# Performance work log

Hardware: AMD Instinct MI355X
Metric: run time of the kernel (lower is better)

Reference implementation:

```python
import jax, jax.numpy as jnp
import numpy as np

H = 16       # query heads
KV = 4       # key/value heads
HD = 256     # head dim
ROPE_THETA = 10000.0
EPS = 1e-6


def _rms_norm(x, w):
    # Gemma RMSNorm over last dim: x / rms * (1 + w), computed in fp32
    xf = x.astype(jnp.float32)
    var = jnp.mean(xf * xf, axis=-1, keepdims=True)
    out = xf * jax.lax.rsqrt(var + EPS) * (1.0 + w.astype(jnp.float32))
    return out.astype(x.dtype)


def _rope_cos_sin(position_ids):
    # cos/sin tables of shape [S, HD]
    inv_freq = 1.0 / (ROPE_THETA ** (jnp.arange(0, HD, 2, dtype=jnp.float32) / HD))
    ang = position_ids.astype(jnp.float32)[:, None] * inv_freq[None, :]  # [S, HD/2]
    emb = jnp.concatenate([ang, ang], axis=-1)                           # [S, HD]
    return jnp.cos(emb), jnp.sin(emb)


def _rotate_half(x):
    x1, x2 = jnp.split(x, 2, axis=-1)
    return jnp.concatenate([-x2, x1], axis=-1)


def _apply_rope(x, cos, sin):
    # x: [B, h, S, HD]; cos/sin: [S, HD] -> broadcast over batch and heads
    c = cos[None, None, :, :]
    s = sin[None, None, :, :]
    return (x * c + _rotate_half(x) * s).astype(x.dtype)


def setup_inputs() -> dict:
    key = jax.random.key(0)
    ks = jax.random.split(key, 8)
    B, S, D = 2, 2048, 2048
    inp = {
        "hidden_states": jax.random.normal(ks[0], (B, S, D), jnp.float32),
        "Wq": jax.random.normal(ks[1], (D, H * HD), jnp.float32) * 0.02,
        "Wk": jax.random.normal(ks[2], (D, KV * HD), jnp.float32) * 0.02,
        "Wv": jax.random.normal(ks[3], (D, KV * HD), jnp.float32) * 0.02,
        "Wo": jax.random.normal(ks[4], (H * HD, D), jnp.float32) * 0.02,
        "q_norm_w": jnp.zeros((HD,), jnp.float32),
        "k_norm_w": jnp.zeros((HD,), jnp.float32),
        "position_ids": jnp.arange(S, dtype=jnp.int32),
    }
    return inp


def reference(hidden_states, Wq, Wk, Wv, Wo, q_norm_w, k_norm_w, position_ids):
    B, S, D = hidden_states.shape
    scale = HD ** -0.5

    # projections -> [B, h, S, HD]
    q = jnp.einsum("bsd,de->bse", hidden_states, Wq).reshape(B, S, H, HD).transpose(0, 2, 1, 3)
    k = jnp.einsum("bsd,de->bse", hidden_states, Wk).reshape(B, S, KV, HD).transpose(0, 2, 1, 3)
    v = jnp.einsum("bsd,de->bse", hidden_states, Wv).reshape(B, S, KV, HD).transpose(0, 2, 1, 3)

    # Gemma per-head RMSNorm on q/k
    q = _rms_norm(q, q_norm_w)
    k = _rms_norm(k, k_norm_w)

    # RoPE
    cos, sin = _rope_cos_sin(position_ids)
    q = _apply_rope(q, cos, sin)
    k = _apply_rope(k, cos, sin)

    # GQA: repeat kv heads to match query heads
    rep = H // KV
    k = jnp.repeat(k, rep, axis=1)  # [B, H, S, HD]
    v = jnp.repeat(v, rep, axis=1)

    # SDPA with causal mask, softmax in fp32
    scores = jnp.einsum("bhqd,bhkd->bhqk", q, k) * scale
    causal = jnp.tril(jnp.ones((S, S), dtype=bool))
    scores = jnp.where(causal[None, None, :, :], scores, jnp.finfo(jnp.float32).min)
    probs = jax.nn.softmax(scores.astype(jnp.float32), axis=-1).astype(q.dtype)
    attn = jnp.einsum("bhqk,bhkd->bhqd", probs, v)  # [B, H, S, HD]

    attn = attn.transpose(0, 2, 1, 3).reshape(B, S, H * HD)
    return jnp.einsum("bse,ed->bsd", attn, Wo)
```

## Files before the change

### kernel.cpp

```cpp
#include <hip/hip_runtime.h>

typedef unsigned short ushort_t;
typedef __bf16 bf16_t;
typedef bf16_t bf16x8 __attribute__((ext_vector_type(8)));
typedef float floatx4 __attribute__((ext_vector_type(4)));
typedef ushort_t ushort4v __attribute__((ext_vector_type(4)));
typedef ushort_t ushort8v __attribute__((ext_vector_type(8)));

static constexpr int B = 2, S = 2048, D = 2048;
static constexpr int H = 16, KVH = 4, HD = 256;

#define DEVFN static __device__ __forceinline__

DEVFN ushort_t f2b(float f) {
  union { float f; unsigned u; } x; x.f = f;
  unsigned r = x.u + 0x7fffu + ((x.u >> 16) & 1u);
  return (ushort_t)(r >> 16);
}
DEVFN float b2f(ushort_t h) {
  union { unsigned u; float f; } x; x.u = ((unsigned)h) << 16;
  return x.f;
}
DEVFN void gll16(const void* g, void* l) {
  __builtin_amdgcn_global_load_lds(
      (const __attribute__((address_space(1))) void*)g,
      (__attribute__((address_space(3))) void*)l, 16, 0, 0);
}

DEVFN void bar() {
  asm volatile("" ::: "memory");
  __builtin_amdgcn_s_barrier();
  asm volatile("" ::: "memory");
}
template <int N>
DEVFN void waitvm() { asm volatile("s_waitcnt vmcnt(%0)" ::"n"(N) : "memory"); }

DEVFN ushort4v norm_rope_row(ushort4v raw, const float* __restrict__ w,
                             const float* __restrict__ tab, int s, float scale, int lane) {
  float v[4];
  float ss = 0.f;
#pragma unroll
  for (int i = 0; i < 4; i++) { v[i] = b2f(raw[i]); ss += v[i] * v[i]; }
#pragma unroll
  for (int m = 1; m < 64; m <<= 1) ss += __shfl_xor(ss, m, 64);
  const float inv = rsqrtf(ss * (1.0f / HD) + 1e-6f);
  float4 wv = *(const float4*)(w + lane * 4);
  float y[4];
  y[0] = v[0] * inv * (1.0f + wv.x);
  y[1] = v[1] * inv * (1.0f + wv.y);
  y[2] = v[2] * inv * (1.0f + wv.z);
  y[3] = v[3] * inv * (1.0f + wv.w);
  float py[4];
#pragma unroll
  for (int i = 0; i < 4; i++) py[i] = __shfl_xor(y[i], 32, 64);
  const bool lo = (lane < 32);
  ushort4v ov;
#pragma unroll
  for (int i = 0; i < 4; i++) {
    int dd = (lane * 4 + i) & 127;
    float2 cs = *(const float2*)(tab + ((size_t)s * 128 + dd) * 2);
    float rot = lo ? -py[i] : py[i];
    ov[i] = f2b((y[i] * cs.x + rot * cs.y) * scale);
  }
  return ov;
}

__global__ void k_cvt_bf16(const float* __restrict__ in, ushort_t* __restrict__ out, int n) {
  int i = (blockIdx.x * 256 + threadIdx.x) * 4;
  if (i >= n) return;
  float4 v = *(const float4*)(in + i);
  ushort4v o;
  o[0] = f2b(v.x); o[1] = f2b(v.y); o[2] = f2b(v.z); o[3] = f2b(v.w);
  *(ushort4v*)(out + i) = o;
}

__global__ void k_transpose_cvt(const float* __restrict__ in, ushort_t* __restrict__ out,
                                int R, int C) {
  __shared__ float tile[64][65];
  const int cb = blockIdx.x * 64, rb = blockIdx.y * 64;
  const int t = threadIdx.x;
  const int l16 = t & 15, g16 = t >> 4;
#pragma unroll
  for (int p = 0; p < 4; p++) {
    const int r = p * 16 + g16;
    float4 v = *(const float4*)(in + (size_t)(rb + r) * C + cb + l16 * 4);
    tile[r][l16 * 4 + 0] = v.x;
    tile[r][l16 * 4 + 1] = v.y;
    tile[r][l16 * 4 + 2] = v.z;
    tile[r][l16 * 4 + 3] = v.w;
  }
  __syncthreads();
#pragma unroll
  for (int p = 0; p < 4; p++) {
    const int c = p * 16 + g16;
    ushort4v o4;
#pragma unroll
    for (int i = 0; i < 4; i++) o4[i] = f2b(tile[l16 * 4 + i][c]);
    *(ushort4v*)(out + (size_t)(cb + c) * R + rb + l16 * 4) = o4;
  }
}

__global__ void k_rope_table(const int* __restrict__ pos_ids, float* __restrict__ tab) {
  int idx = blockIdx.x * 256 + threadIdx.x;
  int s = idx >> 7, dd = idx & 127;
  float ang = (float)pos_ids[s] * exp2f((float)dd * (-13.287712379549449f / 128.0f));
  tab[idx * 2] = cosf(ang);
  tab[idx * 2 + 1] = sinf(ang);
}

DEVFN void stage_tile(const ushort_t* __restrict__ A, const ushort_t* __restrict__ Bt,
                      ushort_t* smb, size_t arow0, size_t brow0, int K, int kt) {
  const int t = threadIdx.x;
  const int rq = t >> 2;
  const int cq = (t & 3) * 8;
#pragma unroll
  for (int i = 0; i < 2; i++) {
    const int cs = cq ^ ((rq & 8) << 1);
    gll16(A + (arow0 + rq) * (size_t)K + kt + i * 32 + cs, smb + i * 4096 + t * 8);
  }
#pragma unroll
  for (int i = 0; i < 4; i++) {
    const int row = ((i & 1) << 7) | rq;
    const int cs = cq ^ ((row & 8) << 1);
    gll16(Bt + (brow0 + row) * (size_t)K + kt + (i >> 1) * 32 + cs,
          smb + 8192 + i * 4096 + t * 8);
  }
}

DEVFN bf16x8 ldsA(const ushort_t* buf, int row, int ks, int lq) {
  const int c = (lq * 8) ^ ((row & 8) << 1);
  return *(const bf16x8*)(buf + ks * 4096 + row * 32 + c);
}
DEVFN bf16x8 ldsB(const ushort_t* buf, int row, int ks, int lq) {
  const int c = (lq * 8) ^ ((row & 8) << 1);
  return *(const bf16x8*)(buf + 8192 + ks * 8192 + row * 32 + c);
}

template <int MODE>
__global__ __launch_bounds__(512, 2)
void k_gemm256(const ushort_t* __restrict__ A, const ushort_t* __restrict__ Bt,
               void* __restrict__ C0, void* __restrict__ C1, void* __restrict__ C2,
               int N, int K) {
  __shared__ ushort_t sm[49152];
  const int tid = threadIdx.x;
  const int lane = tid & 63, wave = tid >> 6;
  const int lr = lane & 15, lq = lane >> 4;
  const int wm = wave >> 2, wn = wave & 3;
  const size_t m0 = (size_t)blockIdx.x * 128;
  const size_t n0 = (size_t)blockIdx.y * 256;

  floatx4 acc[4][4];
#pragma unroll
  for (int i = 0; i < 4; i++)
#pragma unroll
    for (int j = 0; j < 4; j++) acc[i][j] = {0.f, 0.f, 0.f, 0.f};

  const int NT = K >> 6;
  stage_tile(A, Bt, sm, m0, n0, K, 0);
  stage_tile(A, Bt, sm + 24576, m0, n0, K, 64);

  for (int t = 0; t < NT; ++t) {
    ushort_t* bA = sm + (t & 1) * 24576;
    if (t < NT - 1) waitvm<6>(); else waitvm<0>();
    bar();

    bf16x8 a[2][4], bfr[2][4];
#pragma unroll
    for (int ks = 0; ks < 2; ks++) {
#pragma unroll
      for (int m = 0; m < 4; m++) a[ks][m] = ldsA(bA, wm * 64 + m * 16 + lr, ks, lq);
#pragma unroll
      for (int n = 0; n < 4; n++) bfr[ks][n] = ldsB(bA, wn * 64 + n * 16 + lr, ks, lq);
    }
    __builtin_amdgcn_s_setprio(1);
#pragma unroll
    for (int m = 0; m < 4; m++)
#pragma unroll
      for (int n = 0; n < 4; n++)
        acc[m][n] = __builtin_amdgcn_mfma_f32_16x16x32_bf16(a[0][m], bfr[0][n], acc[m][n], 0, 0, 0);
    __builtin_amdgcn_s_setprio(0);
    asm volatile("s_waitcnt lgkmcnt(0)" ::: "memory");
    __builtin_amdgcn_sched_barrier(0);
    bar();
    if (t + 2 < NT) stage_tile(A, Bt, bA, m0, n0, K, (t + 2) * 64);
    __builtin_amdgcn_sched_barrier(0);
    __builtin_amdgcn_s_setprio(1);
#pragma unroll
    for (int m = 0; m < 4; m++)
#pragma unroll
      for (int n = 0; n < 4; n++)
        acc[m][n] = __builtin_amdgcn_mfma_f32_16x16x32_bf16(a[1][m], bfr[1][n], acc[m][n], 0, 0, 0);
    __builtin_amdgcn_s_setprio(0);
  }

  const int colb = (int)n0;
#pragma unroll
  for (int mg = 0; mg < 4; mg++)
#pragma unroll
    for (int ng = 0; ng < 4; ng++) {
      const size_t row0 = m0 + wm * 64 + mg * 16 + lq * 4;
      const int col = colb + wn * 64 + ng * 16 + lr;
      if (MODE == 1) {
#pragma unroll
        for (int r = 0; r < 4; r++)
          ((float*)C0)[(row0 + r) * N + col] = acc[mg][ng][r];
      } else {
        if (colb < 4096) {
#pragma unroll
          for (int r = 0; r < 4; r++)
            ((ushort_t*)C0)[(row0 + r) * 4096 + col] = f2b(acc[mg][ng][r]);
        } else if (colb < 5120) {
#pragma unroll
          for (int r = 0; r < 4; r++)
            ((ushort_t*)C1)[(row0 + r) * 1024 + (col - 4096)] = f2b(acc[mg][ng][r]);
        } else {
          const int ch = col - 5120;
          const int kvh = ch >> 8, chh = ch & 255, f = chh >> 4, lrv = chh & 15;
          const size_t bb = row0 >> 11;
          const int s0 = (int)(row0 & 2047);
          const int tile = s0 >> 6, kh = (s0 >> 5) & 1, lqv = (s0 >> 3) & 3, j0 = s0 & 7;
          ushort4v pk;
#pragma unroll
          for (int r = 0; r < 4; r++) pk[r] = f2b(acc[mg][ng][r]);
          *(ushort4v*)&((ushort_t*)C2)[((bb * KVH + kvh) * (S / 64) + tile) * 16384 +
                                       (size_t)(f * 2 + kh) * 512 +
                                       (size_t)(lqv * 16 + lrv) * 8 + j0] = pk;
        }
      }
    }
}

__global__ void k_norm_rope_k(const ushort_t* __restrict__ Kb, ushort_t* __restrict__ Kf,
                              const float* __restrict__ w, const float* __restrict__ tab) {
  __shared__ ushort_t t[64 * 264];
  const int lane = threadIdx.x & 63, wave = threadIdx.x >> 6;
  const int tile = blockIdx.x, kvh = blockIdx.y, b = blockIdx.z;
#pragma unroll
  for (int rr = 0; rr < 16; rr++) {
    const int row = wave * 16 + rr;
    const int s = tile * 64 + row;
    const ushort_t* p = Kb + ((size_t)(b * S + s) * KVH + kvh) * HD + lane * 4;
    ushort4v raw = *(const ushort4v*)p;
    *(ushort4v*)&t[row * 264 + lane * 4] = norm_rope_row(raw, w, tab, s, 1.0f, lane);
  }
  __syncthreads();
  ushort_t* dst = Kf + ((size_t)(b * KVH + kvh) * (S / 64) + tile) * 16384;
  const int lr = lane & 15, lq = lane >> 4;
#pragma unroll
  for (int q = 0; q < 8; q++) {
    const int c = wave * 8 + q;
    const int nt = c >> 3, ks = c & 7;
    ushort8v v = *(const ushort8v*)&t[(nt * 16 + lr) * 264 + ks * 32 + lq * 8];
    *(ushort8v*)&dst[(size_t)c * 512 + lane * 8] = v;
  }
}

__global__ __launch_bounds__(512, 2)
void k_attn(const ushort_t* __restrict__ Q, const ushort_t* __restrict__ Kf,
            const ushort_t* __restrict__ Vf, ushort_t* __restrict__ O,
            const float* __restrict__ qw, const float* __restrict__ tab) {
  __shared__ ushort_t Ks[2][16384];
  __shared__ ushort_t Vs[2][16384];
  __shared__ ushort_t Ps[8][16 * 72];
  const int lane = threadIdx.x & 63, wave = threadIdx.x >> 6;
  const int lr = lane & 15, lq = lane >> 4;
  const int h = blockIdx.y, b = blockIdx.z;
  const int kvh = h >> 2;
  const size_t kvb = (size_t)(b * KVH + kvh) * (S / 64);

#pragma unroll 1
  for (int half = 0; half < 2; half++) {
    const int qt = half ? (int)blockIdx.x : (S / 128 - 1 - (int)blockIdx.x);
    const int qw0 = qt * 128 + wave * 16;
    const int sq = qw0 + lr;

    bf16x8 qf[8];
    {
      const ushort_t* qp = Q + ((size_t)(b * S + sq) * H + h) * HD + lq * 8;
      ushort8v qr[8];
#pragma unroll
      for (int ks = 0; ks < 8; ks++) qr[ks] = *(const ushort8v*)(qp + ks * 32);
      float ss = 0.f;
#pragma unroll
      for (int ks = 0; ks < 8; ks++)
#pragma unroll
        for (int j = 0; j < 8; j++) { float v = b2f(qr[ks][j]); ss += v * v; }
      ss += __shfl_xor(ss, 16, 64);
      ss += __shfl_xor(ss, 32, 64);
      const float inv = rsqrtf(ss * (1.0f / HD) + 1e-6f);
      const float sc = 0.0625f * 1.4426950408889634f;
#pragma unroll
      for (int c = 0; c < 4; c++) {
        const int d0 = c * 32 + lq * 8;
        float wl[8], wh[8];
        {
          float4 a0 = *(const float4*)(qw + d0);
          float4 a1 = *(const float4*)(qw + d0 + 4);
          float4 a2 = *(const float4*)(qw + d0 + 128);
          float4 a3 = *(const float4*)(qw + d0 + 132);
          wl[0]=a0.x; wl[1]=a0.y; wl[2]=a0.z; wl[3]=a0.w;
          wl[4]=a1.x; wl[5]=a1.y; wl[6]=a1.z; wl[7]=a1.w;
          wh[0]=a2.x; wh[1]=a2.y; wh[2]=a2.z; wh[3]=a2.w;
          wh[4]=a3.x; wh[5]=a3.y; wh[6]=a3.z; wh[7]=a3.w;
        }
        const float* tp = tab + ((size_t)sq * 128 + d0) * 2;
        ushort8v olo, ohi;
#pragma unroll
        for (int j = 0; j < 8; j++) {
          float ylo = b2f(qr[c][j]) * inv * (1.0f + wl[j]);
          float yhi = b2f(qr[c + 4][j]) * inv * (1.0f + wh[j]);
          float2 cs = *(const float2*)(tp + j * 2);
          olo[j] = f2b((ylo * cs.x - yhi * cs.y) * sc);
          ohi[j] = f2b((yhi * cs.x + ylo * cs.y) * sc);
        }
        qf[c] = *reinterpret_cast<bf16x8*>(&olo);
        qf[c + 4] = *reinterpret_cast<bf16x8*>(&ohi);
      }
    }

    floatx4 o[16];
#pragma unroll
    for (int f = 0; f < 16; f++) o[f] = {0.f, 0.f, 0.f, 0.f};
    float m_i[4] = {-1e30f, -1e30f, -1e30f, -1e30f};
    float l_i[4] = {0.f, 0.f, 0.f, 0.f};

    const int ntiles = 2 * qt + 2;
    {
      const ushort_t* tb = Kf + kvb * 16384;
      const ushort_t* vb = Vf + kvb * 16384;
#pragma unroll
      for (int tt = 0; tt < 2; tt++) {
#pragma unroll
        for (int i = 0; i < 4; i++) {
          const int c = wave * 4 + i;
          gll16(tb + (size_t)tt * 16384 + c * 512 + lane * 8, &Ks[tt][c * 512 + lane * 8]);
          gll16(vb + (size_t)tt * 16384 + c * 512 + lane * 8, &Vs[tt][c * 512 + lane * 8]);
        }
      }
    }
    waitvm<8>();
    bar();

    for (int kt = 0; kt < ntiles; kt++) {
      const int kbase = kt * 64;
      const int cur = kt & 1;
      const ushort_t* ksb = Ks[cur];
      const ushort_t* vsb = Vs[cur];

      const int ntmax = min(4, ((qw0 + 15 - kbase) >> 4) + 1);
      floatx4 sacc[4];
      __builtin_amdgcn_s_setprio(1);
#pragma unroll
      for (int nt = 0; nt < 4; nt++) {
        if (nt < ntmax) {
          sacc[nt] = {0.f, 0.f, 0.f, 0.f};
#pragma unroll
          for (int ks = 0; ks < 8; ks++) {
            bf16x8 kf = *(const bf16x8*)&ksb[(nt * 8 + ks) * 512 + lane * 8];
            sacc[nt] = __builtin_amdgcn_mfma_f32_16x16x32_bf16(qf[ks], kf, sacc[nt], 0, 0, 0);
          }
        } else {
          sacc[nt] = {-1e30f, -1e30f, -1e30f, -1e30f};
        }
      }
      __builtin_amdgcn_s_setprio(0);
      if (kbase + 63 > qw0) {
#pragma unroll
        for (int nt = 0; nt < 4; nt++)
          if (nt < ntmax)
#pragma unroll
            for (int r = 0; r < 4; r++)
              if (kbase + nt * 16 + lr > qw0 + lq * 4 + r) sacc[nt][r] = -1e30f;
      }
      float mt[4], alpha[4], rs[4];
#pragma unroll
      for (int r = 0; r < 4; r++)
        mt[r] = fmaxf(fmaxf(sacc[0][r], sacc[1][r]), fmaxf(sacc[2][r], sacc[3][r]));
#pragma unroll
      for (int m = 1; m < 16; m <<= 1)
#pragma unroll
        for (int r = 0; r < 4; r++) mt[r] = fmaxf(mt[r], __shfl_xor(mt[r], m, 64));
#pragma unroll
      for (int r = 0; r < 4; r++) {
        float mn = fmaxf(m_i[r], mt[r]);
        alpha[r] = exp2f(m_i[r] - mn);
        m_i[r] = mn;
      }
#pragma unroll
      for (int nt = 0; nt < 4; nt++)
#pragma unroll
        for (int r = 0; r < 4; r++) sacc[nt][r] = exp2f(sacc[nt][r] - m_i[r]);
#pragma unroll
      for (int r = 0; r < 4; r++)
        rs[r] = (sacc[0][r] + sacc[1][r]) + (sacc[2][r] + sacc[3][r]);
#pragma unroll
      for (int m = 1; m < 16; m <<= 1)
#pragma unroll
        for (int r = 0; r < 4; r++) rs[r] += __shfl_xor(rs[r], m, 64);
#pragma unroll
      for (int r = 0; r < 4; r++) l_i[r] = l_i[r] * alpha[r] + rs[r];
      if (__any((alpha[0] < 1.f) | (alpha[1] < 1.f) | (alpha[2] < 1.f) | (alpha[3] < 1.f))) {
#pragma unroll
        for (int f = 0; f < 16; f++) {
          o[f][0] *= alpha[0]; o[f][1] *= alpha[1];
          o[f][2] *= alpha[2]; o[f][3] *= alpha[3];
        }
      }
      ushort_t* psw = Ps[wave];
#pragma unroll
      for (int nt = 0; nt < 4; nt++)
#pragma unroll
        for (int r = 0; r < 4; r++)
          psw[(lq * 4 + r) * 72 + nt * 16 + lr] = f2b(sacc[nt][r]);
      bf16x8 pf0 = *(const bf16x8*)&psw[lr * 72 + lq * 8];
      bf16x8 pf1 = *(const bf16x8*)&psw[lr * 72 + 32 + lq * 8];
      __builtin_amdgcn_s_setprio(1);
#pragma unroll
      for (int f = 0; f < 16; f++) {
        bf16x8 vf0 = *(const bf16x8*)&vsb[(f * 2 + 0) * 512 + lane * 8];
        o[f] = __builtin_amdgcn_mfma_f32_16x16x32_bf16(pf0, vf0, o[f], 0, 0, 0);
        bf16x8 vf1 = *(const bf16x8*)&vsb[(f * 2 + 1) * 512 + lane * 8];
        o[f] = __builtin_amdgcn_mfma_f32_16x16x32_bf16(pf1, vf1, o[f], 0, 0, 0);
      }
      __builtin_amdgcn_s_setprio(0);

      bar();
      if (kt + 2 < ntiles) {
        const ushort_t* tb = Kf + (kvb + kt + 2) * 16384;
        const ushort_t* vb = Vf + (kvb + kt + 2) * 16384;
#pragma unroll
        for (int i = 0; i < 4; i++) {
          const int c = wave * 4 + i;
          gll16(tb + c * 512 + lane * 8, &Ks[cur][c * 512 + lane * 8]);
          gll16(vb + c * 512 + lane * 8, &Vs[cur][c * 512 + lane * 8]);
        }
        waitvm<8>();
      } else if (kt + 1 < ntiles) {
        waitvm<0>();
      }
      bar();
    }
    float invl[4];
#pragma unroll
    for (int r = 0; r < 4; r++) invl[r] = 1.0f / l_i[r];
#pragma unroll
    for (int f = 0; f < 16; f++)
#pragma unroll
      for (int r = 0; r < 4; r++)
        O[((size_t)(b * S + qw0 + lq * 4 + r) * H + h) * HD + f * 16 + lr] =
            f2b(o[f][r] * invl[r]);
  }
}

extern "C" void kernel_launch(void* const* d_in, const int* in_sizes, int n_in,
                              void* d_out, int out_size, void* d_ws, size_t ws_size,
                              hipStream_t stream) {
  const float* hs = (const float*)d_in[0];
  const float* Wq = (const float*)d_in[1];
  const float* Wk = (const float*)d_in[2];
  const float* Wv = (const float*)d_in[3];
  const float* Wo = (const float*)d_in[4];
  const float* qw = (const float*)d_in[5];
  const float* kw = (const float*)d_in[6];
  const int* pos = (const int*)d_in[7];
  float* out = (float*)d_out;

  char* ws = (char*)d_ws;
  size_t off = 0;
  auto alloc = [&](size_t bytes) {
    void* p = ws + off;
    off += (bytes + 255) & ~(size_t)255;
    return p;
  };
  ushort_t* Xb   = (ushort_t*)alloc((size_t)B * S * D * 2);
  ushort_t* Wqt  = (ushort_t*)alloc((size_t)(H * HD) * D * 2);
  ushort_t* Wkvt = (ushort_t*)alloc((size_t)(2 * KVH * HD) * D * 2);
  ushort_t* Wot  = (ushort_t*)alloc((size_t)D * (H * HD) * 2);
  ushort_t* Qb   = (ushort_t*)alloc((size_t)B * S * H * HD * 2);
  ushort_t* Kf   = (ushort_t*)alloc((size_t)B * S * KVH * HD * 2);
  ushort_t* Vf   = (ushort_t*)alloc((size_t)B * S * KVH * HD * 2);
  ushort_t* Ab   = (ushort_t*)alloc((size_t)B * S * H * HD * 2);
  float*    tab  = (float*)alloc((size_t)S * 128 * 2 * sizeof(float));
  ushort_t* Kb = Ab;

  k_cvt_bf16<<<(B * S * D / 4 + 255) / 256, 256, 0, stream>>>(hs, Xb, B * S * D);
  k_transpose_cvt<<<dim3((H * HD) / 64, D / 64), 256, 0, stream>>>(Wq, Wqt, D, H * HD);
  k_transpose_cvt<<<dim3((KVH * HD) / 64, D / 64), 256, 0, stream>>>(Wk, Wkvt, D, KVH * HD);
  k_transpose_cvt<<<dim3((KVH * HD) / 64, D / 64), 256, 0, stream>>>(
      Wv, Wkvt + (size_t)(KVH * HD) * D, D, KVH * HD);
  k_transpose_cvt<<<dim3(D / 64, (H * HD) / 64), 256, 0, stream>>>(Wo, Wot, H * HD, D);
  k_rope_table<<<S * 128 / 256, 256, 0, stream>>>(pos, tab);

  k_gemm256<0><<<dim3((B * S) / 128, 6144 / 256), 512, 0, stream>>>(
      Xb, Wqt, Qb, Kb, Vf, 6144, D);

  k_norm_rope_k<<<dim3(S / 64, KVH, B), 256, 0, stream>>>(Kb, Kf, kw, tab);

  k_attn<<<dim3(S / 256, H, B), 512, 0, stream>>>(Qb, Kf, Vf, Ab, qw, tab);

  k_gemm256<1><<<dim3((B * S) / 128, D / 256), 512, 0, stream>>>(
      Ab, Wot, out, nullptr, nullptr, D, H * HD);
}
```

Baseline: 546.2 us.

## Shrink attention blocks to 64-row query tiles with split K/V single-buffer pipelining

The attention kernel now uses 256-thread blocks with 64 query rows instead of 512 threads with 128 rows. It replaces the double-buffered K/V tiles in LDS with single buffers, refilling K after QK^T and V after PV so each load overlaps the other half of the work. The grid becomes a flat 512 blocks, ordered so blocks sharing a KV head and batch are adjacent, which should help L2 reuse and raise occupancy through smaller LDS use. The cost is more barriers per tile and less prefetch distance, which can expose load latency.

```diff
diff --git a/kernel.cpp b/kernel.cpp
--- a/kernel.cpp
+++ b/kernel.cpp
@@ -255,24 +255,43 @@
   }
 }
 
-__global__ __launch_bounds__(512, 2)
+__global__ __launch_bounds__(256, 2)
 void k_attn(const ushort_t* __restrict__ Q, const ushort_t* __restrict__ Kf,
             const ushort_t* __restrict__ Vf, ushort_t* __restrict__ O,
             const float* __restrict__ qw, const float* __restrict__ tab) {
-  __shared__ ushort_t Ks[2][16384];
-  __shared__ ushort_t Vs[2][16384];
-  __shared__ ushort_t Ps[8][16 * 72];
+  __shared__ ushort_t Ks[16384];
+  __shared__ ushort_t Vs[16384];
+  __shared__ ushort_t Ps[4][16 * 72];
   const int lane = threadIdx.x & 63, wave = threadIdx.x >> 6;
   const int lr = lane & 15, lq = lane >> 4;
-  const int h = blockIdx.y, b = blockIdx.z;
-  const int kvh = h >> 2;
+  const int lin = blockIdx.x;
+  const int g = lin & 7, j = lin >> 3;
+  const int b = g >> 2, kvh = g & 3;
+  const int h = kvh * 4 + (j >> 4);
+  const int xq = j & 15;
   const size_t kvb = (size_t)(b * KVH + kvh) * (S / 64);
 
 #pragma unroll 1
   for (int half = 0; half < 2; half++) {
-    const int qt = half ? (int)blockIdx.x : (S / 128 - 1 - (int)blockIdx.x);
-    const int qw0 = qt * 128 + wave * 16;
-    const int sq = qw0 + lr;
+    const int qt = half ? xq : (S / 64 - 1 - xq);
+    const int q0 = qt * 64 + wave * 16;
+    const int sq = q0 + lr;
+    const int ntiles = qt + 1;
+
+    {
+      const ushort_t* tb = Kf + kvb * 16384;
+      const ushort_t* vb = Vf + kvb * 16384;
+#pragma unroll
+      for (int i = 0; i < 8; i++) {
+        const int c = wave * 8 + i;
+        gll16(tb + (size_t)c * 512 + lane * 8, &Ks[c * 512 + lane * 8]);
+      }
+#pragma unroll
+      for (int i = 0; i < 8; i++) {
+        const int c = wave * 8 + i;
+        gll16(vb + (size_t)c * 512 + lane * 8, &Vs[c * 512 + lane * 8]);
+      }
+    }
 
     bf16x8 qf[8];
     {
@@ -284,7 +303,7 @@
 #pragma unroll
       for (int ks = 0; ks < 8; ks++)
 #pragma unroll
-        for (int j = 0; j < 8; j++) { float v = b2f(qr[ks][j]); ss += v * v; }
+        for (int jj = 0; jj < 8; jj++) { float v = b2f(qr[ks][jj]); ss += v * v; }
       ss += __shfl_xor(ss, 16, 64);
       ss += __shfl_xor(ss, 32, 64);
       const float inv = rsqrtf(ss * (1.0f / HD) + 1e-6f);
@@ -306,12 +325,12 @@
         const float* tp = tab + ((size_t)sq * 128 + d0) * 2;
         ushort8v olo, ohi;
 #pragma unroll
-        for (int j = 0; j < 8; j++) {
-          float ylo = b2f(qr[c][j]) * inv * (1.0f + wl[j]);
-          float yhi = b2f(qr[c + 4][j]) * inv * (1.0f + wh[j]);
-          float2 cs = *(const float2*)(tp + j * 2);
-          olo[j] = f2b((ylo * cs.x - yhi * cs.y) * sc);
-          ohi[j] = f2b((yhi * cs.x + ylo * cs.y) * sc);
+        for (int jj = 0; jj < 8; jj++) {
+          float ylo = b2f(qr[c][jj]) * inv * (1.0f + wl[jj]);
+          float yhi = b2f(qr[c + 4][jj]) * inv * (1.0f + wh[jj]);
+          float2 cs = *(const float2*)(tp + jj * 2);
+          olo[jj] = f2b((ylo * cs.x - yhi * cs.y) * sc);
+          ohi[jj] = f2b((yhi * cs.x + ylo * cs.y) * sc);
         }
         qf[c] = *reinterpret_cast<bf16x8*>(&olo);
         qf[c + 4] = *reinterpret_cast<bf16x8*>(&ohi);
@@ -324,30 +343,14 @@
     float m_i[4] = {-1e30f, -1e30f, -1e30f, -1e30f};
     float l_i[4] = {0.f, 0.f, 0.f, 0.f};
 
-    const int ntiles = 2 * qt + 2;
-    {
-      const ushort_t* tb = Kf + kvb * 16384;
-      const ushort_t* vb = Vf + kvb * 16384;
-#pragma unroll
-      for (int tt = 0; tt < 2; tt++) {
-#pragma unroll
-        for (int i = 0; i < 4; i++) {
-          const int c = wave * 4 + i;
-          gll16(tb + (size_t)tt * 16384 + c * 512 + lane * 8, &Ks[tt][c * 512 + lane * 8]);
-          gll16(vb + (size_t)tt * 16384 + c * 512 + lane * 8, &Vs[tt][c * 512 + lane * 8]);
-        }
-      }
-    }
     waitvm<8>();
     bar();
 
     for (int kt = 0; kt < ntiles; kt++) {
       const int kbase = kt * 64;
-      const int cur = kt & 1;
-      const ushort_t* ksb = Ks[cur];
-      const ushort_t* vsb = Vs[cur];
-
-      const int ntmax = min(4, ((qw0 + 15 - kbase) >> 4) + 1);
+      const bool last = (kt == ntiles - 1);
+
+      const int ntmax = min(4, ((q0 + 15 - kbase) >> 4) + 1);
       floatx4 sacc[4];
       __builtin_amdgcn_s_setprio(1);
 #pragma unroll
@@ -356,7 +359,7 @@
           sacc[nt] = {0.f, 0.f, 0.f, 0.f};
 #pragma unroll
           for (int ks = 0; ks < 8; ks++) {
-            bf16x8 kf = *(const bf16x8*)&ksb[(nt * 8 + ks) * 512 + lane * 8];
+            bf16x8 kf = *(const bf16x8*)&Ks[(nt * 8 + ks) * 512 + lane * 8];
             sacc[nt] = __builtin_amdgcn_mfma_f32_16x16x32_bf16(qf[ks], kf, sacc[nt], 0, 0, 0);
           }
         } else {
@@ -364,13 +367,25 @@
         }
       }
       __builtin_amdgcn_s_setprio(0);
-      if (kbase + 63 > qw0) {
+      asm volatile("s_waitcnt lgkmcnt(0)" ::: "memory");
+      __builtin_amdgcn_sched_barrier(0);
+      bar();
+      if (!last) {
+        const ushort_t* tb = Kf + (kvb + kt + 1) * 16384;
+#pragma unroll
+        for (int i = 0; i < 8; i++) {
+          const int c = wave * 8 + i;
+          gll16(tb + (size_t)c * 512 + lane * 8, &Ks[c * 512 + lane * 8]);
+        }
+      }
+
+      if (kbase + 63 > q0) {
 #pragma unroll
         for (int nt = 0; nt < 4; nt++)
           if (nt < ntmax)
 #pragma unroll
             for (int r = 0; r < 4; r++)
-              if (kbase + nt * 16 + lr > qw0 + lq * 4 + r) sacc[nt][r] = -1e30f;
+              if (kbase + nt * 16 + lr > q0 + lq * 4 + r) sacc[nt][r] = -1e30f;
       }
       float mt[4], alpha[4], rs[4];
 #pragma unroll
@@ -414,32 +429,37 @@
           psw[(lq * 4 + r) * 72 + nt * 16 + lr] = f2b(sacc[nt][r]);
       bf16x8 pf0 = *(const bf16x8*)&psw[lr * 72 + lq * 8];
       bf16x8 pf1 = *(const bf16x8*)&psw[lr * 72 + 32 + lq * 8];
+
+      if (last) waitvm<0>(); else waitvm<8>();
+      bar();
+
       __builtin_amdgcn_s_setprio(1);
 #pragma unroll
       for (int f = 0; f < 16; f++) {
-        bf16x8 vf0 = *(const bf16x8*)&vsb[(f * 2 + 0) * 512 + lane * 8];
+        bf16x8 vf0 = *(const bf16x8*)&Vs[(f * 2 + 0) * 512 + lane * 8];
         o[f] = __builtin_amdgcn_mfma_f32_16x16x32_bf16(pf0, vf0, o[f], 0, 0, 0);
-        bf16x8 vf1 = *(const bf16x8*)&vsb[(f * 2 + 1) * 512 + lane * 8];
+        bf16x8 vf1 = *(const bf16x8*)&Vs[(f * 2 + 1) * 512 + lane * 8];
         o[f] = __builtin_amdgcn_mfma_f32_16x16x32_bf16(pf1, vf1, o[f], 0, 0, 0);
       }
       __builtin_amdgcn_s_setprio(0);
 
-      bar();
-      if (kt + 2 < ntiles) {
-        const ushort_t* tb = Kf + (kvb + kt + 2) * 16384;
-        const ushort_t* vb = Vf + (kvb + kt + 2) * 16384;
-#pragma unroll
-        for (int i = 0; i < 4; i++) {
-          const int c = wave * 4 + i;
-          gll16(tb + c * 512 + lane * 8, &Ks[cur][c * 512 + lane * 8]);
-          gll16(vb + c * 512 + lane * 8, &Vs[cur][c * 512 + lane * 8]);
+      if (!last) {
+        asm volatile("s_waitcnt lgkmcnt(0)" ::: "memory");
+        __builtin_amdgcn_sched_barrier(0);
+        bar();
+        const ushort_t* vb = Vf + (kvb + kt + 1) * 16384;
+#pragma unroll
+        for (int i = 0; i < 8; i++) {
+          const int c = wave * 8 + i;
+          gll16(vb + (size_t)c * 512 + lane * 8, &Vs[c * 512 + lane * 8]);
         }
         waitvm<8>();
-      } else if (kt + 1 < ntiles) {
-        waitvm<0>();
-      }
-      bar();
+        bar();
+      }
     }
+    asm volatile("s_waitcnt lgkmcnt(0)" ::: "memory");
+    bar();
+
     float invl[4];
 #pragma unroll
     for (int r = 0; r < 4; r++) invl[r] = 1.0f / l_i[r];
@@ -447,7 +467,7 @@
     for (int f = 0; f < 16; f++)
 #pragma unroll
       for (int r = 0; r < 4; r++)
-        O[((size_t)(b * S + qw0 + lq * 4 + r) * H + h) * HD + f * 16 + lr] =
+        O[((size_t)(b * S + q0 + lq * 4 + r) * H + h) * HD + f * 16 + lr] =
             f2b(o[f][r] * invl[r]);
   }
 }
@@ -496,7 +516,7 @@
 
   k_norm_rope_k<<<dim3(S / 64, KVH, B), 256, 0, stream>>>(Kb, Kf, kw, tab);
 
-  k_attn<<<dim3(S / 256, H, B), 512, 0, stream>>>(Qb, Kf, Vf, Ab, qw, tab);
+  k_attn<<<512, 256, 0, stream>>>(Qb, Kf, Vf, Ab, qw, tab);
 
   k_gemm256<1><<<dim3((B * S) / 128, D / 256), 512, 0, stream>>>(
       Ab, Wot, out, nullptr, nullptr, D, H * HD);
```

New measurement: 527.7 us. -3.4%, faster.
